# Optimization experiments

Hardware: AMD Instinct MI355X
Metric: run time of the kernel (lower is better)

## Reference

```python
import jax, jax.numpy as jnp
import numpy as np

HIDDEN = 1024
N_HEADS = 16
D_HEAD = HIDDEN // N_HEADS
B, S = 4, 2048


def setup_inputs() -> dict:
    key = jax.random.key(0)
    ks = jax.random.split(key, 7)
    scale = 1.0 / np.sqrt(D_HEAD)
    return {
        "sequences": jax.random.normal(ks[0], (B, S, HIDDEN), dtype=jnp.float32),
        "Wq": jax.random.normal(ks[1], (N_HEADS, D_HEAD, D_HEAD), dtype=jnp.float32) * scale,
        "bq": jax.random.normal(ks[2], (N_HEADS, D_HEAD), dtype=jnp.float32) * 0.02,
        "Wk": jax.random.normal(ks[3], (N_HEADS, D_HEAD, D_HEAD), dtype=jnp.float32) * scale,
        "bk": jax.random.normal(ks[4], (N_HEADS, D_HEAD), dtype=jnp.float32) * 0.02,
        "Wv": jax.random.normal(ks[5], (N_HEADS, D_HEAD, D_HEAD), dtype=jnp.float32) * scale,
        "bv": jax.random.normal(ks[6], (N_HEADS, D_HEAD), dtype=jnp.float32) * 0.02,
    }


def reference(sequences, Wq, bq, Wk, bk, Wv, bv):
    # sequences: [B, S, hidden]; split hidden into per-head slices -> [B, S, H, d]
    x = sequences.reshape(B, S, N_HEADS, D_HEAD)
    # per-head Linear: y = x @ W^T + b (torch nn.Linear convention)
    q = jnp.einsum("bshd,hed->bshe", x, Wq) + bq  # [B,S,H,d]
    k = jnp.einsum("bshd,hed->bshe", x, Wk) + bk
    v = jnp.einsum("bshd,hed->bshe", x, Wv) + bv
    scores = jnp.einsum("bqhd,bkhd->bhqk", q, k) / np.sqrt(D_HEAD)  # [B,H,S,S]
    attn = jax.nn.softmax(scores, axis=-1)
    out = jnp.einsum("bhqk,bkhd->bqhd", attn, v)  # [B,S,H,d]
    # hstack over heads == concat along feature dim
    return out.reshape(B, S, HIDDEN)
```

## Files before the change

kernel.cpp:

```cpp
#include <hip/hip_runtime.h>
#include <hip/hip_bf16.h>

#define NB 4
#define NS 2048
#define NH 16
#define ND 64
#define NHID 1024
#define NT (NS / 64)
#define QSCALE 0.18033688011112042f

typedef __bf16 bf16x8 __attribute__((ext_vector_type(8)));
typedef _Float16 f16x8 __attribute__((ext_vector_type(8)));
typedef _Float16 f16x4 __attribute__((ext_vector_type(4)));
typedef __fp16 h16x2 __attribute__((ext_vector_type(2)));
typedef float f32x4 __attribute__((ext_vector_type(4)));

#define GLDS16(g, l)                                                      \
  __builtin_amdgcn_global_load_lds(                                       \
      (const __attribute__((address_space(1))) void*)(g),                 \
      (__attribute__((address_space(3))) void*)(l), 16, 0, 0)

__device__ __forceinline__ bf16x8 cvt8(const float* __restrict__ p) {
  float4 f0 = *(const float4*)p;
  float4 f1 = *(const float4*)(p + 4);
  bf16x8 v;
  v[0] = (__bf16)f0.x; v[1] = (__bf16)f0.y; v[2] = (__bf16)f0.z; v[3] = (__bf16)f0.w;
  v[4] = (__bf16)f1.x; v[5] = (__bf16)f1.y; v[6] = (__bf16)f1.z; v[7] = (__bf16)f1.w;
  return v;
}

__global__ void wcvt(const float* __restrict__ Wq, const float* __restrict__ Wk,
                     const float* __restrict__ Wv, __bf16* __restrict__ Wb) {
  const int M = NH * ND * ND;
  int i = blockIdx.x * 256 + threadIdx.x;
  float v;
  if (i < M)            v = Wq[i] * QSCALE;
  else if (i < 2 * M)   v = Wk[i - M];
  else                  v = Wv[i - 2 * M];
  Wb[i] = (__bf16)v;
}

__global__ __launch_bounds__(256, 2) void qkv_proj(
    const float* __restrict__ x, const __bf16* __restrict__ Wb,
    const float* __restrict__ bq, const float* __restrict__ bk,
    const float* __restrict__ bv,
    __bf16* __restrict__ qs, __bf16* __restrict__ ks, _Float16* __restrict__ vt)
{
  __shared__ __align__(16) unsigned short tiles[4][64 * 72];

  const int bid = blockIdx.x;
  const int hg = bid & 3;
  const int s0 = ((bid >> 2) & 31) * 64;
  const int b  = bid >> 7;
  const int tid  = threadIdx.x;
  const int w    = tid >> 6;
  const int lane = tid & 63;
  const int l16  = lane & 15;
  const int quad = lane >> 4;
  const int h  = hg * 4 + w;
  const int bh = b * NH + h;

  unsigned short* tile = tiles[w];
  __bf16*   tb16 = (__bf16*)tile;
  _Float16* tf16 = (_Float16*)tile;

  bf16x8 aX[4][2];
#pragma unroll
  for (int tb = 0; tb < 4; ++tb) {
    const float* xrow = x + ((size_t)(b * NS + s0 + tb * 16 + l16)) * NHID + h * ND;
#pragma unroll
    for (int k2 = 0; k2 < 2; ++k2)
      aX[tb][k2] = cvt8(xrow + k2 * 32 + quad * 8);
  }

#pragma unroll
  for (int mat = 0; mat < 3; ++mat) {
    const __bf16* Wm = Wb + ((size_t)(mat * NH + h)) * ND * ND;
    const float* bm = (mat == 0) ? bq : (mat == 1) ? bk : bv;

    f32x4 acc[4][4];
#pragma unroll
    for (int nb = 0; nb < 4; ++nb) {
      const int e = nb * 16 + l16;
      bf16x8 w0 = *(const bf16x8*)(Wm + e * ND + quad * 8);
      bf16x8 w1 = *(const bf16x8*)(Wm + e * ND + 32 + quad * 8);
#pragma unroll
      for (int tbk = 0; tbk < 4; ++tbk) {
        f32x4 a = {0.f, 0.f, 0.f, 0.f};
        a = __builtin_amdgcn_mfma_f32_16x16x32_bf16(aX[tbk][0], w0, a, 0, 0, 0);
        a = __builtin_amdgcn_mfma_f32_16x16x32_bf16(aX[tbk][1], w1, a, 0, 0, 0);
        acc[nb][tbk] = a;
      }
    }

    if (mat < 2) {
#pragma unroll
      for (int nb = 0; nb < 4; ++nb) {
        float bias = bm[h * ND + nb * 16 + l16] * ((mat == 0) ? QSCALE : 1.0f);
#pragma unroll
        for (int tbk = 0; tbk < 4; ++tbk)
#pragma unroll
          for (int r = 0; r < 4; ++r)
            tb16[(tbk * 16 + quad * 4 + r) * 72 + nb * 16 + l16] =
                (__bf16)(acc[nb][tbk][r] + bias);
      }
#pragma unroll
      for (int p = 0; p < 8; ++p) {
        int idx = p * 64 + lane, row = idx >> 3, c = idx & 7;
        bf16x8 v8 = *(const bf16x8*)(tb16 + row * 72 + c * 8);
        if (mat == 0)
          *(bf16x8*)(qs + ((size_t)bh * NS + s0 + row) * ND + c * 8) = v8;
        else
          *(bf16x8*)(ks + ((size_t)bh * NS + s0 + row) * ND + ((c ^ (row & 7)) * 8)) = v8;
      }
    } else {
#pragma unroll
      for (int nb = 0; nb < 4; ++nb) {
        float bias = bm[h * ND + nb * 16 + l16];
#pragma unroll
        for (int tbk = 0; tbk < 4; ++tbk) {
          union { h16x2 h2[2]; uint2 u2; } pv;
          pv.h2[0] = __builtin_amdgcn_cvt_pkrtz(acc[nb][tbk][0] + bias,
                                                acc[nb][tbk][1] + bias);
          pv.h2[1] = __builtin_amdgcn_cvt_pkrtz(acc[nb][tbk][2] + bias,
                                                acc[nb][tbk][3] + bias);
          *(uint2*)&tf16[(nb * 16 + l16) * 72 + tbk * 16 + quad * 4] = pv.u2;
        }
      }
#pragma unroll
      for (int p = 0; p < 8; ++p) {
        int idx = p * 64 + lane, row = idx >> 3, c = idx & 7;
        int K0 = 32 * (c >> 2) + 4 * (c & 3);
        union { f16x4 v4[2]; f16x8 v8; } u;
        u.v4[0] = *(const f16x4*)(tf16 + row * 72 + K0);
        u.v4[1] = *(const f16x4*)(tf16 + row * 72 + K0 + 16);
        *(f16x8*)(vt + ((size_t)bh * ND + row) * NS + s0 + ((c ^ (row & 7)) * 8)) = u.v8;
      }
    }
  }
}

__global__ __launch_bounds__(256, 4) void attn(
    const __bf16* __restrict__ qs, const __bf16* __restrict__ ks,
    const _Float16* __restrict__ vt, float* __restrict__ out)
{
  __shared__ __align__(16) __bf16   KT[2][64 * 64];
  __shared__ __align__(16) _Float16 VT[2][64 * 64];

  const int bid = blockIdx.x;
  const int qt = bid >> 6;
  const int h  = bid & 15;
  const int b  = (bid >> 4) & 3;
  const int bh = b * NH + h;
  const int tid  = threadIdx.x;
  const int w    = tid >> 6;
  const int lane = tid & 63;
  const int l16  = lane & 15;
  const int quad = lane >> 4;
  const int swz  = l16 & 7;
  const int qw   = qt * 128 + w * 32;

  const __bf16*   Kb = ks + (size_t)bh * NS * ND;
  const _Float16* Vb = vt + (size_t)bh * ND * NS;

  bf16x8 Qf[2][2];
#pragma unroll
  for (int qb = 0; qb < 2; ++qb)
#pragma unroll
    for (int k2 = 0; k2 < 2; ++k2)
      Qf[qb][k2] = *(const bf16x8*)(qs + ((size_t)bh * NS + qw + qb * 16 + l16) * ND +
                                    k2 * 32 + quad * 8);

  f32x4 acc[2][4];
#pragma unroll
  for (int qb = 0; qb < 2; ++qb)
#pragma unroll
    for (int mb = 0; mb < 4; ++mb) acc[qb][mb] = (f32x4){0.f, 0.f, 0.f, 0.f};
  f32x4 lacc[2] = {(f32x4){0.f, 0.f, 0.f, 0.f}, (f32x4){0.f, 0.f, 0.f, 0.f}};
  const f16x8 onesf = {(_Float16)1.f, (_Float16)1.f, (_Float16)1.f, (_Float16)1.f,
                       (_Float16)1.f, (_Float16)1.f, (_Float16)1.f, (_Float16)1.f};

#pragma unroll
  for (int p = 0; p < 2; ++p) {
    int i = (w * 2 + p) * 64 + lane;
    GLDS16(Kb + (size_t)0 * 4096 + i * 8, &KT[0][i * 8]);
    int row = i >> 3, cc = i & 7;
    GLDS16(Vb + (size_t)row * NS + 0 * 64 + cc * 8, &VT[0][i * 8]);
  }

  for (int kt = 0; kt < NT; ++kt) {
    const int cur = kt & 1;
    __syncthreads();
    if (kt + 1 < NT) {
      const int nxt = cur ^ 1;
#pragma unroll
      for (int p = 0; p < 2; ++p) {
        int i = (w * 2 + p) * 64 + lane;
        GLDS16(Kb + (size_t)(kt + 1) * 4096 + i * 8, &KT[nxt][i * 8]);
        int row = i >> 3, cc = i & 7;
        GLDS16(Vb + (size_t)row * NS + (kt + 1) * 64 + cc * 8, &VT[nxt][i * 8]);
      }
    }

    const __bf16*   Kl = KT[cur];
    const _Float16* Vl = VT[cur];

    f32x4 sc[2][4];
    __builtin_amdgcn_s_setprio(1);
#pragma unroll
    for (int kb = 0; kb < 4; ++kb) {
      const __bf16* krow = Kl + (kb * 16 + l16) * 64;
      bf16x8 Kf0 = *(const bf16x8*)(krow + ((quad ^ swz) * 8));
      bf16x8 Kf1 = *(const bf16x8*)(krow + (((4 + quad) ^ swz) * 8));
#pragma unroll
      for (int qb = 0; qb < 2; ++qb) {
        f32x4 s = {0.f, 0.f, 0.f, 0.f};
        s = __builtin_amdgcn_mfma_f32_16x16x32_bf16(Kf0, Qf[qb][0], s, 0, 0, 0);
        s = __builtin_amdgcn_mfma_f32_16x16x32_bf16(Kf1, Qf[qb][1], s, 0, 0, 0);
        sc[qb][kb] = s;
      }
    }
    __builtin_amdgcn_s_setprio(0);

    f16x8 bp8[2][2];
#pragma unroll
    for (int qb = 0; qb < 2; ++qb) {
#pragma unroll
      for (int g = 0; g < 2; ++g) {
        float p0 = __builtin_amdgcn_exp2f(sc[qb][2 * g][0]);
        float p1 = __builtin_amdgcn_exp2f(sc[qb][2 * g][1]);
        float p2 = __builtin_amdgcn_exp2f(sc[qb][2 * g][2]);
        float p3 = __builtin_amdgcn_exp2f(sc[qb][2 * g][3]);
        float p4 = __builtin_amdgcn_exp2f(sc[qb][2 * g + 1][0]);
        float p5 = __builtin_amdgcn_exp2f(sc[qb][2 * g + 1][1]);
        float p6 = __builtin_amdgcn_exp2f(sc[qb][2 * g + 1][2]);
        float p7 = __builtin_amdgcn_exp2f(sc[qb][2 * g + 1][3]);
        union { h16x2 v2[4]; f16x8 v8; } u;
        u.v2[0] = __builtin_amdgcn_cvt_pkrtz(p0, p1);
        u.v2[1] = __builtin_amdgcn_cvt_pkrtz(p2, p3);
        u.v2[2] = __builtin_amdgcn_cvt_pkrtz(p4, p5);
        u.v2[3] = __builtin_amdgcn_cvt_pkrtz(p6, p7);
        bp8[qb][g] = u.v8;
      }
    }

    __builtin_amdgcn_s_setprio(1);
#pragma unroll
    for (int g = 0; g < 2; ++g) {
#pragma unroll
      for (int mb = 0; mb < 4; ++mb) {
        f16x8 Vf = *(const f16x8*)(Vl + (mb * 16 + l16) * 64 + (((g * 4 + quad) ^ swz)) * 8);
#pragma unroll
        for (int qb = 0; qb < 2; ++qb)
          acc[qb][mb] = __builtin_amdgcn_mfma_f32_16x16x32_f16(Vf, bp8[qb][g], acc[qb][mb], 0, 0, 0);
      }
#pragma unroll
      for (int qb = 0; qb < 2; ++qb)
        lacc[qb] = __builtin_amdgcn_mfma_f32_16x16x32_f16(onesf, bp8[qb][g], lacc[qb], 0, 0, 0);
    }
    __builtin_amdgcn_s_setprio(0);
  }

#pragma unroll
  for (int qb = 0; qb < 2; ++qb) {
    float invl = 1.0f / lacc[qb][0];
    const size_t orow = ((size_t)(b * NS) + qw + qb * 16 + l16) * NHID + h * ND;
#pragma unroll
    for (int mb = 0; mb < 4; ++mb) {
      float4 o4 = {acc[qb][mb][0] * invl, acc[qb][mb][1] * invl,
                   acc[qb][mb][2] * invl, acc[qb][mb][3] * invl};
      *(float4*)(out + orow + mb * 16 + quad * 4) = o4;
    }
  }
}

extern "C" void kernel_launch(void* const* d_in, const int* in_sizes, int n_in,
                              void* d_out, int out_size, void* d_ws, size_t ws_size,
                              hipStream_t stream) {
  const float* x  = (const float*)d_in[0];
  const float* Wq = (const float*)d_in[1];
  const float* bq = (const float*)d_in[2];
  const float* Wk = (const float*)d_in[3];
  const float* bk = (const float*)d_in[4];
  const float* Wv = (const float*)d_in[5];
  const float* bv = (const float*)d_in[6];
  float* out = (float*)d_out;

  const size_t per = (size_t)NB * NH * NS * ND;
  __bf16* qs   = (__bf16*)d_ws;
  __bf16* ksb  = qs + per;
  _Float16* vt = (_Float16*)(ksb + per);
  __bf16* Wb   = (__bf16*)(vt + per);

  wcvt<<<768, 256, 0, stream>>>(Wq, Wk, Wv, Wb);
  qkv_proj<<<NB * (NS / 64) * (NH / 4), 256, 0, stream>>>(x, Wb, bq, bk, bv, qs, ksb, vt);
  attn<<<16 * NB * NH, 256, 0, stream>>>(qs, ksb, vt, out);
}
```

Measured before the change: 178.0 us.

## Fold weight conversion into projection kernel and halve projection tile size

Removes the separate weight-conversion launch: each projection wave now reads the fp32 weights directly and converts and scales them to bf16 in registers. The projection tile shrinks from 64 to 32 sequence rows, doubling the grid to 1024 blocks and raising launch bounds to 4 blocks per CU for more parallelism. The V-transpose store is reworked to keep the swizzled layout at half-tile granularity. In exchange, weights are converted redundantly in every block and fp32 weight traffic per block doubles.

```diff
diff --git a/kernel.cpp b/kernel.cpp
--- a/kernel.cpp
+++ b/kernel.cpp
@@ -29,29 +29,31 @@
   return v;
 }
 
-__global__ void wcvt(const float* __restrict__ Wq, const float* __restrict__ Wk,
-                     const float* __restrict__ Wv, __bf16* __restrict__ Wb) {
-  const int M = NH * ND * ND;
-  int i = blockIdx.x * 256 + threadIdx.x;
-  float v;
-  if (i < M)            v = Wq[i] * QSCALE;
-  else if (i < 2 * M)   v = Wk[i - M];
-  else                  v = Wv[i - 2 * M];
-  Wb[i] = (__bf16)v;
-}
-
-__global__ __launch_bounds__(256, 2) void qkv_proj(
-    const float* __restrict__ x, const __bf16* __restrict__ Wb,
+__device__ __forceinline__ bf16x8 cvt8s(const float* __restrict__ p, float s) {
+  float4 f0 = *(const float4*)p;
+  float4 f1 = *(const float4*)(p + 4);
+  bf16x8 v;
+  v[0] = (__bf16)(f0.x * s); v[1] = (__bf16)(f0.y * s);
+  v[2] = (__bf16)(f0.z * s); v[3] = (__bf16)(f0.w * s);
+  v[4] = (__bf16)(f1.x * s); v[5] = (__bf16)(f1.y * s);
+  v[6] = (__bf16)(f1.z * s); v[7] = (__bf16)(f1.w * s);
+  return v;
+}
+
+__global__ __launch_bounds__(256, 4) void qkv_proj(
+    const float* __restrict__ x,
+    const float* __restrict__ Wq, const float* __restrict__ Wk,
+    const float* __restrict__ Wv,
     const float* __restrict__ bq, const float* __restrict__ bk,
     const float* __restrict__ bv,
     __bf16* __restrict__ qs, __bf16* __restrict__ ks, _Float16* __restrict__ vt)
 {
-  __shared__ __align__(16) unsigned short tiles[4][64 * 72];
+  __shared__ __align__(16) unsigned short tiles[4][2304];
 
   const int bid = blockIdx.x;
   const int hg = bid & 3;
-  const int s0 = ((bid >> 2) & 31) * 64;
-  const int b  = bid >> 7;
+  const int s0 = ((bid >> 2) & 63) * 32;
+  const int b  = bid >> 8;
   const int tid  = threadIdx.x;
   const int w    = tid >> 6;
   const int lane = tid & 63;
@@ -59,14 +61,16 @@
   const int quad = lane >> 4;
   const int h  = hg * 4 + w;
   const int bh = b * NH + h;
+  const int g0  = s0 & ~63;
+  const int h64 = (s0 >> 5) & 1;
 
   unsigned short* tile = tiles[w];
   __bf16*   tb16 = (__bf16*)tile;
   _Float16* tf16 = (_Float16*)tile;
 
-  bf16x8 aX[4][2];
-#pragma unroll
-  for (int tb = 0; tb < 4; ++tb) {
+  bf16x8 aX[2][2];
+#pragma unroll
+  for (int tb = 0; tb < 2; ++tb) {
     const float* xrow = x + ((size_t)(b * NS + s0 + tb * 16 + l16)) * NHID + h * ND;
 #pragma unroll
     for (int k2 = 0; k2 < 2; ++k2)
@@ -75,17 +79,18 @@
 
 #pragma unroll
   for (int mat = 0; mat < 3; ++mat) {
-    const __bf16* Wm = Wb + ((size_t)(mat * NH + h)) * ND * ND;
+    const float* Wm = ((mat == 0) ? Wq : (mat == 1) ? Wk : Wv) + (size_t)h * ND * ND;
     const float* bm = (mat == 0) ? bq : (mat == 1) ? bk : bv;
-
-    f32x4 acc[4][4];
+    const float wsc = (mat == 0) ? QSCALE : 1.0f;
+
+    f32x4 acc[4][2];
 #pragma unroll
     for (int nb = 0; nb < 4; ++nb) {
       const int e = nb * 16 + l16;
-      bf16x8 w0 = *(const bf16x8*)(Wm + e * ND + quad * 8);
-      bf16x8 w1 = *(const bf16x8*)(Wm + e * ND + 32 + quad * 8);
-#pragma unroll
-      for (int tbk = 0; tbk < 4; ++tbk) {
+      bf16x8 w0 = cvt8s(Wm + e * ND + quad * 8, wsc);
+      bf16x8 w1 = cvt8s(Wm + e * ND + 32 + quad * 8, wsc);
+#pragma unroll
+      for (int tbk = 0; tbk < 2; ++tbk) {
         f32x4 a = {0.f, 0.f, 0.f, 0.f};
         a = __builtin_amdgcn_mfma_f32_16x16x32_bf16(aX[tbk][0], w0, a, 0, 0, 0);
         a = __builtin_amdgcn_mfma_f32_16x16x32_bf16(aX[tbk][1], w1, a, 0, 0, 0);
@@ -96,16 +101,16 @@
     if (mat < 2) {
 #pragma unroll
       for (int nb = 0; nb < 4; ++nb) {
-        float bias = bm[h * ND + nb * 16 + l16] * ((mat == 0) ? QSCALE : 1.0f);
-#pragma unroll
-        for (int tbk = 0; tbk < 4; ++tbk)
+        float bias = bm[h * ND + nb * 16 + l16] * wsc;
+#pragma unroll
+        for (int tbk = 0; tbk < 2; ++tbk)
 #pragma unroll
           for (int r = 0; r < 4; ++r)
             tb16[(tbk * 16 + quad * 4 + r) * 72 + nb * 16 + l16] =
                 (__bf16)(acc[nb][tbk][r] + bias);
       }
 #pragma unroll
-      for (int p = 0; p < 8; ++p) {
+      for (int p = 0; p < 4; ++p) {
         int idx = p * 64 + lane, row = idx >> 3, c = idx & 7;
         bf16x8 v8 = *(const bf16x8*)(tb16 + row * 72 + c * 8);
         if (mat == 0)
@@ -118,23 +123,24 @@
       for (int nb = 0; nb < 4; ++nb) {
         float bias = bm[h * ND + nb * 16 + l16];
 #pragma unroll
-        for (int tbk = 0; tbk < 4; ++tbk) {
+        for (int tbk = 0; tbk < 2; ++tbk) {
           union { h16x2 h2[2]; uint2 u2; } pv;
           pv.h2[0] = __builtin_amdgcn_cvt_pkrtz(acc[nb][tbk][0] + bias,
                                                 acc[nb][tbk][1] + bias);
           pv.h2[1] = __builtin_amdgcn_cvt_pkrtz(acc[nb][tbk][2] + bias,
                                                 acc[nb][tbk][3] + bias);
-          *(uint2*)&tf16[(nb * 16 + l16) * 72 + tbk * 16 + quad * 4] = pv.u2;
+          *(uint2*)&tf16[(nb * 16 + l16) * 36 + tbk * 16 + quad * 4] = pv.u2;
         }
       }
 #pragma unroll
-      for (int p = 0; p < 8; ++p) {
-        int idx = p * 64 + lane, row = idx >> 3, c = idx & 7;
-        int K0 = 32 * (c >> 2) + 4 * (c & 3);
+      for (int p = 0; p < 4; ++p) {
+        int idx = p * 64 + lane, row = idx >> 2, cl = idx & 3;
+        int clog = h64 * 4 + cl;
         union { f16x4 v4[2]; f16x8 v8; } u;
-        u.v4[0] = *(const f16x4*)(tf16 + row * 72 + K0);
-        u.v4[1] = *(const f16x4*)(tf16 + row * 72 + K0 + 16);
-        *(f16x8*)(vt + ((size_t)bh * ND + row) * NS + s0 + ((c ^ (row & 7)) * 8)) = u.v8;
+        u.v4[0] = *(const f16x4*)(tf16 + row * 36 + 4 * cl);
+        u.v4[1] = *(const f16x4*)(tf16 + row * 36 + 16 + 4 * cl);
+        *(f16x8*)(vt + ((size_t)bh * ND + row) * NS + g0 +
+                  ((clog ^ (row & 7)) * 8)) = u.v8;
       }
     }
   }
@@ -290,9 +296,8 @@
   __bf16* qs   = (__bf16*)d_ws;
   __bf16* ksb  = qs + per;
   _Float16* vt = (_Float16*)(ksb + per);
-  __bf16* Wb   = (__bf16*)(vt + per);
-
-  wcvt<<<768, 256, 0, stream>>>(Wq, Wk, Wv, Wb);
-  qkv_proj<<<NB * (NS / 64) * (NH / 4), 256, 0, stream>>>(x, Wb, bq, bk, bv, qs, ksb, vt);
+
+  qkv_proj<<<NB * (NS / 32) * (NH / 4), 256, 0, stream>>>(
+      x, Wq, Wk, Wv, bq, bk, bv, qs, ksb, vt);
   attn<<<16 * NB * NH, 256, 0, stream>>>(qs, ksb, vt, out);
 }
```

Result: slower. 188.0 us (+5.6%).
